# Performance work log

Measured on AMD Instinct MI355X. Metric: run time of the kernel, lower is better.

## Reference

```python
import jax, jax.numpy as jnp
import numpy as np


def _component_indices(d, j):
    # Butterfly component at level j has block size k = d >> j.
    k = d >> j
    half = k // 2
    base = np.arange(d // k) * k                       # block starts
    p = (base[:, None] + np.arange(half)[None, :]).reshape(-1)  # [d//2]
    q = p + half
    return p, q


def butterfly_rotation(thetas, d):
    """Compose m = log2(d) butterfly components: R = B(d,d) @ B(d,d/2) @ ... @ B(d,2).
    thetas: [m, d//2] Givens angles per component (block-major order as in torch)."""
    m = thetas.shape[0]
    R = jnp.eye(d, dtype=thetas.dtype)
    for j in range(m):
        p, q = _component_indices(d, j)
        c = jnp.cos(thetas[j])
        s = jnp.sin(thetas[j])
        C = jnp.eye(d, dtype=thetas.dtype)
        C = C.at[p, p].set(c)
        C = C.at[q, q].set(c)
        C = C.at[p, q].set(-s)
        C = C.at[q, p].set(s)
        R = R @ C
    return R


def setup_inputs() -> dict:
    key = jax.random.key(0)
    ks = jax.random.split(key, 8)
    N, D_IN, D_OUT, R = 16384, 4096, 4096, 1024
    M = 10  # log2(R)
    return {
        "x": jax.random.normal(ks[0], (N, D_IN), dtype=jnp.float32),
        "W": jax.random.normal(ks[1], (D_OUT, D_IN), dtype=jnp.float32) * 0.02,
        "bias": jax.random.normal(ks[2], (D_OUT,), dtype=jnp.float32) * 0.02,
        "U": jax.random.normal(ks[3], (D_OUT, R), dtype=jnp.float32) * 0.02,
        "S": jax.random.uniform(ks[4], (R,), dtype=jnp.float32),
        "V": jax.random.normal(ks[5], (R, D_IN), dtype=jnp.float32) * 0.02,
        "thetas_u": jax.random.normal(ks[6], (M, R // 2), dtype=jnp.float32) * 0.1,
        "thetas_v": jax.random.normal(ks[7], (M, R // 2), dtype=jnp.float32) * 0.1,
    }


def reference(x, W, bias, U, S, V, thetas_u, thetas_v):
    r = S.shape[0]
    R_U = butterfly_rotation(thetas_u, r)  # [r, r]
    R_V = butterfly_rotation(thetas_v, r)  # [r, r]
    # base_layer(x)
    base = x @ W.T + bias                  # [N, out]
    # adapter: x @ V^T @ R_V @ diag(S) @ R_U^T @ U^T
    h = (x @ V.T) @ R_V                    # [N, r]
    h = h * S                              # diag(S)
    delta = (h @ R_U.T) @ U.T              # [N, out]
    return base + delta
```

## Files before the change

### kernel.cpp

```cpp
#include <hip/hip_runtime.h>
#include <cstdint>
#include <cstddef>


typedef __bf16 bf16x8 __attribute__((ext_vector_type(8)));
typedef float floatx4 __attribute__((ext_vector_type(4)));
typedef unsigned short ushortx8 __attribute__((ext_vector_type(8)));

__device__ __forceinline__ unsigned short f2bf(float f) {
    unsigned int u = __builtin_bit_cast(unsigned int, f);
    u += 0x7FFFu + ((u >> 16) & 1u);
    return (unsigned short)(u >> 16);
}

__device__ __forceinline__ void gld_lds16(const void* g, void* l) {
    __builtin_amdgcn_global_load_lds(
        (const __attribute__((address_space(1))) void*)g,
        (__attribute__((address_space(3))) void*)l,
        16, 0, 0);
}

__global__ __launch_bounds__(256) void butterfly_rows_kernel(
    const float* __restrict__ thetas_v, const float* __restrict__ thetas_u,
    const float* __restrict__ S,
    unsigned short* __restrict__ RVsb, unsigned short* __restrict__ RUb)
{
    const int d = 1024;
    __shared__ float w[1024];
    const int b   = blockIdx.x;
    const int mat = b >> 10;
    const int row = b & 1023;
    const float* th = mat ? thetas_u : thetas_v;
    const int t = threadIdx.x;

    for (int i = t; i < d; i += 256) w[i] = (i == row) ? 1.f : 0.f;
    __syncthreads();

    for (int j = 0; j < 10; ++j) {
        const int sh = 9 - j;
        const int halfm1 = (1 << sh) - 1;
        for (int i = t; i < d / 2; i += 256) {
            const int blk = i >> sh;
            const int off = i & halfm1;
            const int p = (blk << (sh + 1)) + off;
            const int q = p + (halfm1 + 1);
            const float theta = th[j * (d / 2) + i];
            float s, c;
            __sincosf(theta, &s, &c);
            const float wp = w[p], wq = w[q];
            w[p] = c * wp + s * wq;
            w[q] = -s * wp + c * wq;
        }
        __syncthreads();
    }

    if (mat == 0) {
        for (int i = t; i < d; i += 256) RVsb[row * d + i] = f2bf(w[i] * S[i]);
    } else {
        for (int i = t; i < d; i += 256) RUb[row * d + i] = f2bf(w[i]);
    }
}

__global__ __launch_bounds__(256) void cvt_f32_bf16_x8(
    const float* __restrict__ src, unsigned short* __restrict__ dst)
{
    const size_t i = ((size_t)blockIdx.x * 256 + threadIdx.x) * 8;
    float4 a = *(const float4*)(src + i);
    float4 b = *(const float4*)(src + i + 4);
    ushortx8 o;
    o[0] = f2bf(a.x); o[1] = f2bf(a.y); o[2] = f2bf(a.z); o[3] = f2bf(a.w);
    o[4] = f2bf(b.x); o[5] = f2bf(b.y); o[6] = f2bf(b.z); o[7] = f2bf(b.w);
    *(ushortx8*)(dst + i) = o;
}

__global__ __launch_bounds__(256) void transpose_to_bf16(
    const float* __restrict__ src, unsigned short* __restrict__ dst,
    int rows, int cols)
{
    __shared__ float tile[32][33];
    const int tx = threadIdx.x & 31, ty = threadIdx.x >> 5;
    const int c0 = blockIdx.x * 32, r0 = blockIdx.y * 32;
    for (int i = 0; i < 32; i += 8)
        tile[ty + i][tx] = src[(size_t)(r0 + ty + i) * cols + c0 + tx];
    __syncthreads();
    for (int i = 0; i < 32; i += 8)
        dst[(size_t)(c0 + ty + i) * rows + r0 + tx] = f2bf(tile[tx][ty + i]);
}

template <int EPI>
__global__ __launch_bounds__(256) void gemm_nt(
    const unsigned short* __restrict__ A,
    const unsigned short* __restrict__ B,
    float* __restrict__ Cf,
    unsigned short* __restrict__ Cb,
    const float* __restrict__ extra,
    int M, int N, int K)
{
    __shared__ __align__(16) unsigned short As[128 * 32];
    __shared__ __align__(16) unsigned short Bs[128 * 32];

    const int tid  = threadIdx.x;
    const int lane = tid & 63;
    const int wave = tid >> 6;
    const int wm = wave >> 1, wn = wave & 1;

    const int m0 = blockIdx.y * 128;
    const int n0 = blockIdx.x * 128;

    const int srow = wave * 32 + (lane >> 2);
    const int scol = (lane & 3) * 8;

    const unsigned short* gA = A + (size_t)(m0 + srow) * K + scol;
    const unsigned short* gB = B + (size_t)(n0 + srow) * K + scol;
    unsigned short* lA = As + wave * 32 * 32;
    unsigned short* lB = Bs + wave * 32 * 32;

    floatx4 acc[4][4];
#pragma unroll
    for (int i = 0; i < 4; ++i)
#pragma unroll
        for (int j = 0; j < 4; ++j) acc[i][j] = (floatx4)0.f;

    const int ar = lane & 15;
    const int ak = (lane >> 4) * 8;

    for (int kk = 0; kk < K; kk += 32) {
        gld_lds16(gA + kk, lA);
        gld_lds16(gA + kk + (size_t)16 * K, lA + 512);
        gld_lds16(gB + kk, lB);
        gld_lds16(gB + kk + (size_t)16 * K, lB + 512);
        __syncthreads();

        bf16x8 af[4], bfr[4];
#pragma unroll
        for (int tm = 0; tm < 4; ++tm)
            af[tm] = __builtin_bit_cast(bf16x8,
                *(const ushortx8*)&As[(wm * 64 + tm * 16 + ar) * 32 + ak]);
#pragma unroll
        for (int tn = 0; tn < 4; ++tn)
            bfr[tn] = __builtin_bit_cast(bf16x8,
                *(const ushortx8*)&Bs[(wn * 64 + tn * 16 + ar) * 32 + ak]);
#pragma unroll
        for (int tm = 0; tm < 4; ++tm)
#pragma unroll
            for (int tn = 0; tn < 4; ++tn)
                acc[tm][tn] = __builtin_amdgcn_mfma_f32_16x16x32_bf16(
                    af[tm], bfr[tn], acc[tm][tn], 0, 0, 0);
        __syncthreads();
    }

#pragma unroll
    for (int tm = 0; tm < 4; ++tm) {
#pragma unroll
        for (int tn = 0; tn < 4; ++tn) {
#pragma unroll
            for (int r = 0; r < 4; ++r) {
                const int row = m0 + wm * 64 + tm * 16 + (lane >> 4) * 4 + r;
                const int col = n0 + wn * 64 + tn * 16 + (lane & 15);
                const float v = acc[tm][tn][r];
                if (EPI == 1) {
                    Cf[(size_t)row * N + col] = v + extra[col];
                } else if (EPI == 2) {
                    Cb[(size_t)row * N + col] = f2bf(v);
                } else {
                    Cb[(size_t)row * N + col] = f2bf(v + extra[(size_t)row * N + col]);
                }
            }
        }
    }
}

template <int EPI>
__global__ __launch_bounds__(512, 2) void gemm256(
    const unsigned short* __restrict__ A,
    const unsigned short* __restrict__ B,
    float* __restrict__ Cf,
    unsigned short* __restrict__ Cb,
    const float* __restrict__ extra,
    int M, int N, int K, int swz_on)
{
    __shared__ __align__(16) unsigned short As[2][256 * 64];
    __shared__ __align__(16) unsigned short Bs[2][256 * 64];

    const int tid  = threadIdx.x;
    const int lane = tid & 63;
    const int wave = tid >> 6;
    const int wm = wave >> 2;
    const int wn = wave & 3;

    int bx = blockIdx.x, by = blockIdx.y;
    if (swz_on) {
        const int gx  = gridDim.x;
        const int nwg = gx * gridDim.y;
        const int f   = by * gx + bx;
        const int g   = (f & 7) * (nwg >> 3) + (f >> 3);
        bx = g % gx;
        by = g / gx;
    }
    const int m0 = by * 256;
    const int n0 = bx * 256;

    const int srow  = tid >> 3;
    const int scolb = (tid & 7) << 4;
    const int scol  = (scolb ^ ((srow & 7) << 4)) >> 1;

    const unsigned short* gA = A + (size_t)(m0 + srow) * K + scol;
    const unsigned short* gB = B + (size_t)(n0 + srow) * K + scol;
    const int ldsoff = wave << 10;
    const size_t rowstep = (size_t)64 * K;

    const int fr   = lane & 15;
    const int fk2  = ((lane >> 4) & 3) << 4;
    const int swz  = (fr & 7) << 4;
    const int ca0  = fk2 ^ swz;
    const int ca1  = (64 + fk2) ^ swz;
    const int arow = (wm * 128 + fr) << 7;
    const int brow = (wn * 64 + fr) << 7;

    floatx4 acc[8][4];
#pragma unroll
    for (int i = 0; i < 8; ++i)
#pragma unroll
        for (int j = 0; j < 4; ++j) acc[i][j] = (floatx4)0.f;

    const int nkt = K >> 6;

    {
        char* la = (char*)&As[0][0] + ldsoff;
        char* lb = (char*)&Bs[0][0] + ldsoff;
#pragma unroll
        for (int j = 0; j < 4; ++j) gld_lds16(gA + j * rowstep, la + j * 8192);
#pragma unroll
        for (int j = 0; j < 4; ++j) gld_lds16(gB + j * rowstep, lb + j * 8192);
    }

    for (int t = 0; t < nkt; ++t) {
        if (t + 1 < nkt) {
            const unsigned short* a = gA + (size_t)(t + 1) * 64;
            const unsigned short* b = gB + (size_t)(t + 1) * 64;
            char* la = (char*)&As[(t + 1) & 1][0] + ldsoff;
            char* lb = (char*)&Bs[(t + 1) & 1][0] + ldsoff;
#pragma unroll
            for (int j = 0; j < 4; ++j) gld_lds16(a + j * rowstep, la + j * 8192);
#pragma unroll
            for (int j = 0; j < 4; ++j) gld_lds16(b + j * rowstep, lb + j * 8192);
            __builtin_amdgcn_sched_barrier(0);
            asm volatile("s_waitcnt vmcnt(8)" ::: "memory");
        } else {
            asm volatile("s_waitcnt vmcnt(0)" ::: "memory");
        }
        __builtin_amdgcn_s_barrier();
        __builtin_amdgcn_sched_barrier(0);

        const char* ab = (const char*)&As[t & 1][0];
        const char* bb = (const char*)&Bs[t & 1][0];

        bf16x8 af[4][2], b0[2][2], b1[2][2];

#pragma unroll
        for (int mf = 0; mf < 4; ++mf) {
            af[mf][0] = __builtin_bit_cast(bf16x8, *(const ushortx8*)(ab + arow + (mf << 11) + ca0));
            af[mf][1] = __builtin_bit_cast(bf16x8, *(const ushortx8*)(ab + arow + (mf << 11) + ca1));
        }
#pragma unroll
        for (int nf = 0; nf < 2; ++nf) {
            b0[nf][0] = __builtin_bit_cast(bf16x8, *(const ushortx8*)(bb + brow + (nf << 11) + ca0));
            b0[nf][1] = __builtin_bit_cast(bf16x8, *(const ushortx8*)(bb + brow + (nf << 11) + ca1));
        }
        __builtin_amdgcn_s_setprio(1);
#pragma unroll
        for (int mf = 0; mf < 4; ++mf)
#pragma unroll
            for (int nf = 0; nf < 2; ++nf) {
                acc[mf][nf] = __builtin_amdgcn_mfma_f32_16x16x32_bf16(af[mf][0], b0[nf][0], acc[mf][nf], 0, 0, 0);
                acc[mf][nf] = __builtin_amdgcn_mfma_f32_16x16x32_bf16(af[mf][1], b0[nf][1], acc[mf][nf], 0, 0, 0);
            }
        __builtin_amdgcn_s_setprio(0);

#pragma unroll
        for (int nf = 0; nf < 2; ++nf) {
            b1[nf][0] = __builtin_bit_cast(bf16x8, *(const ushortx8*)(bb + brow + 4096 + (nf << 11) + ca0));
            b1[nf][1] = __builtin_bit_cast(bf16x8, *(const ushortx8*)(bb + brow + 4096 + (nf << 11) + ca1));
        }
        __builtin_amdgcn_s_setprio(1);
#pragma unroll
        for (int mf = 0; mf < 4; ++mf)
#pragma unroll
            for (int nf = 0; nf < 2; ++nf) {
                acc[mf][2 + nf] = __builtin_amdgcn_mfma_f32_16x16x32_bf16(af[mf][0], b1[nf][0], acc[mf][2 + nf], 0, 0, 0);
                acc[mf][2 + nf] = __builtin_amdgcn_mfma_f32_16x16x32_bf16(af[mf][1], b1[nf][1], acc[mf][2 + nf], 0, 0, 0);
            }
        __builtin_amdgcn_s_setprio(0);

#pragma unroll
        for (int mf = 0; mf < 4; ++mf) {
            af[mf][0] = __builtin_bit_cast(bf16x8, *(const ushortx8*)(ab + arow + 8192 + (mf << 11) + ca0));
            af[mf][1] = __builtin_bit_cast(bf16x8, *(const ushortx8*)(ab + arow + 8192 + (mf << 11) + ca1));
        }
        __builtin_amdgcn_s_setprio(1);
#pragma unroll
        for (int mf = 0; mf < 4; ++mf)
#pragma unroll
            for (int nf = 0; nf < 2; ++nf) {
                acc[4 + mf][2 + nf] = __builtin_amdgcn_mfma_f32_16x16x32_bf16(af[mf][0], b1[nf][0], acc[4 + mf][2 + nf], 0, 0, 0);
                acc[4 + mf][2 + nf] = __builtin_amdgcn_mfma_f32_16x16x32_bf16(af[mf][1], b1[nf][1], acc[4 + mf][2 + nf], 0, 0, 0);
            }
        __builtin_amdgcn_s_setprio(0);

#pragma unroll
        for (int nf = 0; nf < 2; ++nf) {
            b0[nf][0] = __builtin_bit_cast(bf16x8, *(const ushortx8*)(bb + brow + (nf << 11) + ca0));
            b0[nf][1] = __builtin_bit_cast(bf16x8, *(const ushortx8*)(bb + brow + (nf << 11) + ca1));
        }
        __builtin_amdgcn_s_setprio(1);
#pragma unroll
        for (int mf = 0; mf < 4; ++mf)
#pragma unroll
            for (int nf = 0; nf < 2; ++nf) {
                acc[4 + mf][nf] = __builtin_amdgcn_mfma_f32_16x16x32_bf16(af[mf][0], b0[nf][0], acc[4 + mf][nf], 0, 0, 0);
                acc[4 + mf][nf] = __builtin_amdgcn_mfma_f32_16x16x32_bf16(af[mf][1], b0[nf][1], acc[4 + mf][nf], 0, 0, 0);
            }
        __builtin_amdgcn_s_setprio(0);

        __builtin_amdgcn_sched_barrier(0);
        asm volatile("" ::: "memory");
        __builtin_amdgcn_s_barrier();
    }

    const int er = wm * 128 + ((lane >> 4) << 2);
    const int ec = wn * 64 + (lane & 15);
#pragma unroll
    for (int mfg = 0; mfg < 8; ++mfg) {
#pragma unroll
        for (int nfg = 0; nfg < 4; ++nfg) {
#pragma unroll
            for (int r = 0; r < 4; ++r) {
                const int row = m0 + er + mfg * 16 + r;
                const int col = n0 + ec + nfg * 16;
                const float v = acc[mfg][nfg][r];
                if (EPI == 1) {
                    Cf[(size_t)row * N + col] = v + extra[col];
                } else {
                    Cb[(size_t)row * N + col] = f2bf(v + extra[(size_t)row * N + col]);
                }
            }
        }
    }
    (void)M;
}

extern "C" void kernel_launch(void* const* d_in, const int* in_sizes, int n_in,
                              void* d_out, int out_size, void* d_ws, size_t ws_size,
                              hipStream_t stream)
{
    const int NB = 16384, DIN = 4096, DOUT = 4096, R = 1024;

    const float* x    = (const float*)d_in[0];
    const float* W    = (const float*)d_in[1];
    const float* bias = (const float*)d_in[2];
    const float* U    = (const float*)d_in[3];
    const float* S    = (const float*)d_in[4];
    const float* V    = (const float*)d_in[5];
    const float* th_u = (const float*)d_in[6];
    const float* th_v = (const float*)d_in[7];
    float* out = (float*)d_out;

    char* ws = (char*)d_ws;
    size_t off = 0;
    auto alloc = [&](size_t bytes) {
        char* p = ws + off;
        off += (bytes + 255) & ~(size_t)255;
        return p;
    };
    unsigned short* Xb   = (unsigned short*)alloc((size_t)NB * DIN * 2);
    unsigned short* Wctb = (unsigned short*)alloc((size_t)DOUT * DIN * 2);
    unsigned short* RVsb = (unsigned short*)alloc((size_t)R * R * 2);
    unsigned short* RUb  = (unsigned short*)alloc((size_t)R * R * 2);
    unsigned short* Tb   = (unsigned short*)alloc((size_t)R * R * 2);
    unsigned short* Ub   = (unsigned short*)alloc((size_t)DOUT * R * 2);
    unsigned short* Gb   = (unsigned short*)alloc((size_t)DOUT * R * 2);
    unsigned short* Vtb  = (unsigned short*)alloc((size_t)DIN * R * 2);
    if (off > ws_size) return;

    butterfly_rows_kernel<<<2048, 256, 0, stream>>>(th_v, th_u, S, RVsb, RUb);

    cvt_f32_bf16_x8<<<(NB * (size_t)DIN) / 2048, 256, 0, stream>>>(x, Xb);
    cvt_f32_bf16_x8<<<((size_t)DOUT * R) / 2048, 256, 0, stream>>>(U, Ub);
    transpose_to_bf16<<<dim3(DIN / 32, R / 32), 256, 0, stream>>>(V, Vtb, R, DIN);

    gemm_nt<2><<<dim3(R / 128, R / 128), 256, 0, stream>>>(
        RVsb, RUb, nullptr, Tb, nullptr, R, R, R);

    gemm_nt<2><<<dim3(R / 128, DOUT / 128), 256, 0, stream>>>(
        Ub, Tb, nullptr, Gb, nullptr, DOUT, R, R);

    gemm256<3><<<dim3(DIN / 256, DOUT / 256), 512, 0, stream>>>(
        Gb, Vtb, nullptr, Wctb, W, DOUT, DIN, R, 0);

    gemm256<1><<<dim3(DOUT / 256, NB / 256), 512, 0, stream>>>(
        Xb, Wctb, out, nullptr, bias, NB, DOUT, DIN, 1);
}
```

Baseline: 1.202 ms.

## Split 256x256 GEMM tile into quadrant halves with staggered per-half prefetch

The 256x256 bf16 GEMM kernel now keeps A and B in LDS as two 128-row halves per buffer. Each wave's fragments are remapped to interleaved 64x32 sub-tiles inside each half. Loads for the next k-tile are issued one half at a time between the four MFMA phases, with partial vmcnt waits and barriers, so global-to-LDS traffic overlaps compute more finely and each phase only waits for the half it needs. This adds several extra workgroup barriers per k-iteration and more complex wait-count bookkeeping, which could cause stalls or ordering hazards.

Measured after the change: 1.142 ms. 5.0% less time.

```diff
diff --git a/kernel.cpp b/kernel.cpp
--- a/kernel.cpp
+++ b/kernel.cpp
@@ -19,6 +19,12 @@
         (__attribute__((address_space(3))) void*)l,
         16, 0, 0);
 }
+
+__device__ __forceinline__ bf16x8 ldsv(const char* p) {
+    return __builtin_bit_cast(bf16x8, *(const ushortx8*)p);
+}
+
+#define MFMA_BF16(a, b, c) __builtin_amdgcn_mfma_f32_16x16x32_bf16((a), (b), (c), 0, 0, 0)
 
 __global__ __launch_bounds__(256) void butterfly_rows_kernel(
     const float* __restrict__ thetas_v, const float* __restrict__ thetas_u,
@@ -144,8 +150,7 @@
         for (int tm = 0; tm < 4; ++tm)
 #pragma unroll
             for (int tn = 0; tn < 4; ++tn)
-                acc[tm][tn] = __builtin_amdgcn_mfma_f32_16x16x32_bf16(
-                    af[tm], bfr[tn], acc[tm][tn], 0, 0, 0);
+                acc[tm][tn] = MFMA_BF16(af[tm], bfr[tn], acc[tm][tn]);
         __syncthreads();
     }
 
@@ -179,8 +184,8 @@
     const float* __restrict__ extra,
     int M, int N, int K, int swz_on)
 {
-    __shared__ __align__(16) unsigned short As[2][256 * 64];
-    __shared__ __align__(16) unsigned short Bs[2][256 * 64];
+    __shared__ __align__(16) unsigned short As[2][2][128][64];
+    __shared__ __align__(16) unsigned short Bs[2][2][128][64];
 
     const int tid  = threadIdx.x;
     const int lane = tid & 63;
@@ -203,19 +208,32 @@
     const int srow  = tid >> 3;
     const int scolb = (tid & 7) << 4;
     const int scol  = (scolb ^ ((srow & 7) << 4)) >> 1;
-
     const unsigned short* gA = A + (size_t)(m0 + srow) * K + scol;
     const unsigned short* gB = B + (size_t)(n0 + srow) * K + scol;
-    const int ldsoff = wave << 10;
-    const size_t rowstep = (size_t)64 * K;
-
-    const int fr   = lane & 15;
-    const int fk2  = ((lane >> 4) & 3) << 4;
-    const int swz  = (fr & 7) << 4;
-    const int ca0  = fk2 ^ swz;
-    const int ca1  = (64 + fk2) ^ swz;
-    const int arow = (wm * 128 + fr) << 7;
-    const int brow = (wn * 64 + fr) << 7;
+    char* lA = (char*)As + (wave << 10);
+    char* lB = (char*)Bs + (wave << 10);
+    const size_t rs64 = (size_t)64 * K;
+
+    auto stA = [&](int t1, int h) {
+        const unsigned short* s = gA + (size_t)h * 2 * rs64 + (size_t)t1 * 64;
+        char* l = lA + (t1 & 1) * 32768 + h * 16384;
+        gld_lds16(s, l);
+        gld_lds16(s + rs64, l + 8192);
+    };
+    auto stB = [&](int t1, int h) {
+        const unsigned short* s = gB + (size_t)h * 2 * rs64 + (size_t)t1 * 64;
+        char* l = lB + (t1 & 1) * 32768 + h * 16384;
+        gld_lds16(s, l);
+        gld_lds16(s + rs64, l + 8192);
+    };
+
+    const int fr  = lane & 15;
+    const int kg  = lane >> 4;
+    const int swz = (fr & 7) << 4;
+    const int ca0 = (kg << 4) ^ swz;
+    const int ca1 = (64 + (kg << 4)) ^ swz;
+    const int arb = (wm * 64 + fr) * 128;
+    const int brb = (wn * 32 + fr) * 128;
 
     floatx4 acc[8][4];
 #pragma unroll
@@ -225,127 +243,127 @@
 
     const int nkt = K >> 6;
 
-    {
-        char* la = (char*)&As[0][0] + ldsoff;
-        char* lb = (char*)&Bs[0][0] + ldsoff;
-#pragma unroll
-        for (int j = 0; j < 4; ++j) gld_lds16(gA + j * rowstep, la + j * 8192);
-#pragma unroll
-        for (int j = 0; j < 4; ++j) gld_lds16(gB + j * rowstep, lb + j * 8192);
-    }
+    stA(0, 0); stB(0, 0); stB(0, 1); stA(0, 1);
+    asm volatile("s_waitcnt vmcnt(4)" ::: "memory");
+    __builtin_amdgcn_s_barrier();
+    __builtin_amdgcn_sched_barrier(0);
 
     for (int t = 0; t < nkt; ++t) {
-        if (t + 1 < nkt) {
-            const unsigned short* a = gA + (size_t)(t + 1) * 64;
-            const unsigned short* b = gB + (size_t)(t + 1) * 64;
-            char* la = (char*)&As[(t + 1) & 1][0] + ldsoff;
-            char* lb = (char*)&Bs[(t + 1) & 1][0] + ldsoff;
-#pragma unroll
-            for (int j = 0; j < 4; ++j) gld_lds16(a + j * rowstep, la + j * 8192);
-#pragma unroll
-            for (int j = 0; j < 4; ++j) gld_lds16(b + j * rowstep, lb + j * 8192);
-            __builtin_amdgcn_sched_barrier(0);
-            asm volatile("s_waitcnt vmcnt(8)" ::: "memory");
-        } else {
-            asm volatile("s_waitcnt vmcnt(0)" ::: "memory");
-        }
-        __builtin_amdgcn_s_barrier();
-        __builtin_amdgcn_sched_barrier(0);
-
-        const char* ab = (const char*)&As[t & 1][0];
-        const char* bb = (const char*)&Bs[t & 1][0];
+        const bool stg = (t + 1 < nkt);
+        const char* Ad = (const char*)As + (t & 1) * 32768;
+        const char* Bd = (const char*)Bs + (t & 1) * 32768;
 
         bf16x8 af[4][2], b0[2][2], b1[2][2];
 
 #pragma unroll
         for (int mf = 0; mf < 4; ++mf) {
-            af[mf][0] = __builtin_bit_cast(bf16x8, *(const ushortx8*)(ab + arow + (mf << 11) + ca0));
-            af[mf][1] = __builtin_bit_cast(bf16x8, *(const ushortx8*)(ab + arow + (mf << 11) + ca1));
+            af[mf][0] = ldsv(Ad + arb + mf * 2048 + ca0);
+            af[mf][1] = ldsv(Ad + arb + mf * 2048 + ca1);
         }
 #pragma unroll
         for (int nf = 0; nf < 2; ++nf) {
-            b0[nf][0] = __builtin_bit_cast(bf16x8, *(const ushortx8*)(bb + brow + (nf << 11) + ca0));
-            b0[nf][1] = __builtin_bit_cast(bf16x8, *(const ushortx8*)(bb + brow + (nf << 11) + ca1));
-        }
+            b0[nf][0] = ldsv(Bd + brb + nf * 2048 + ca0);
+            b0[nf][1] = ldsv(Bd + brb + nf * 2048 + ca1);
+        }
+        if (stg) { stA(t + 1, 0); asm volatile("s_waitcnt vmcnt(4)" ::: "memory"); }
+        else     {                asm volatile("s_waitcnt vmcnt(2)" ::: "memory"); }
+        __builtin_amdgcn_s_barrier();
+        asm volatile("s_waitcnt lgkmcnt(0)" ::: "memory");
+        __builtin_amdgcn_sched_barrier(0);
         __builtin_amdgcn_s_setprio(1);
 #pragma unroll
         for (int mf = 0; mf < 4; ++mf)
 #pragma unroll
             for (int nf = 0; nf < 2; ++nf) {
-                acc[mf][nf] = __builtin_amdgcn_mfma_f32_16x16x32_bf16(af[mf][0], b0[nf][0], acc[mf][nf], 0, 0, 0);
-                acc[mf][nf] = __builtin_amdgcn_mfma_f32_16x16x32_bf16(af[mf][1], b0[nf][1], acc[mf][nf], 0, 0, 0);
+                acc[mf][nf] = MFMA_BF16(af[mf][0], b0[nf][0], acc[mf][nf]);
+                acc[mf][nf] = MFMA_BF16(af[mf][1], b0[nf][1], acc[mf][nf]);
             }
         __builtin_amdgcn_s_setprio(0);
+        __builtin_amdgcn_s_barrier();
+        __builtin_amdgcn_sched_barrier(0);
 
 #pragma unroll
         for (int nf = 0; nf < 2; ++nf) {
-            b1[nf][0] = __builtin_bit_cast(bf16x8, *(const ushortx8*)(bb + brow + 4096 + (nf << 11) + ca0));
-            b1[nf][1] = __builtin_bit_cast(bf16x8, *(const ushortx8*)(bb + brow + 4096 + (nf << 11) + ca1));
-        }
+            b1[nf][0] = ldsv(Bd + 16384 + brb + nf * 2048 + ca0);
+            b1[nf][1] = ldsv(Bd + 16384 + brb + nf * 2048 + ca1);
+        }
+        if (stg) { stB(t + 1, 0); asm volatile("s_waitcnt vmcnt(4)" ::: "memory"); }
+        else     {                asm volatile("s_waitcnt vmcnt(0)" ::: "memory"); }
+        __builtin_amdgcn_s_barrier();
+        asm volatile("s_waitcnt lgkmcnt(0)" ::: "memory");
+        __builtin_amdgcn_sched_barrier(0);
         __builtin_amdgcn_s_setprio(1);
 #pragma unroll
         for (int mf = 0; mf < 4; ++mf)
 #pragma unroll
             for (int nf = 0; nf < 2; ++nf) {
-                acc[mf][2 + nf] = __builtin_amdgcn_mfma_f32_16x16x32_bf16(af[mf][0], b1[nf][0], acc[mf][2 + nf], 0, 0, 0);
-                acc[mf][2 + nf] = __builtin_amdgcn_mfma_f32_16x16x32_bf16(af[mf][1], b1[nf][1], acc[mf][2 + nf], 0, 0, 0);
+                acc[mf][2 + nf] = MFMA_BF16(af[mf][0], b1[nf][0], acc[mf][2 + nf]);
+                acc[mf][2 + nf] = MFMA_BF16(af[mf][1], b1[nf][1], acc[mf][2 + nf]);
             }
         __builtin_amdgcn_s_setprio(0);
+        __builtin_amdgcn_s_barrier();
+        __builtin_amdgcn_sched_barrier(0);
 
 #pragma unroll
         for (int mf = 0; mf < 4; ++mf) {
-            af[mf][0] = __builtin_bit_cast(bf16x8, *(const ushortx8*)(ab + arow + 8192 + (mf << 11) + ca0));
-            af[mf][1] = __builtin_bit_cast(bf16x8, *(const ushortx8*)(ab + arow + 8192 + (mf << 11) + ca1));
-        }
+            af[mf][0] = ldsv(Ad + 16384 + arb + mf * 2048 + ca0);
+            af[mf][1] = ldsv(Ad + 16384 + arb + mf * 2048 + ca1);
+        }
+        if (stg) stB(t + 1, 1);
+        asm volatile("" ::: "memory");
+        __builtin_amdgcn_s_barrier();
+        asm volatile("s_waitcnt lgkmcnt(0)" ::: "memory");
+        __builtin_amdgcn_sched_barrier(0);
         __builtin_amdgcn_s_setprio(1);
 #pragma unroll
         for (int mf = 0; mf < 4; ++mf)
 #pragma unroll
             for (int nf = 0; nf < 2; ++nf) {
-                acc[4 + mf][2 + nf] = __builtin_amdgcn_mfma_f32_16x16x32_bf16(af[mf][0], b1[nf][0], acc[4 + mf][2 + nf], 0, 0, 0);
-                acc[4 + mf][2 + nf] = __builtin_amdgcn_mfma_f32_16x16x32_bf16(af[mf][1], b1[nf][1], acc[4 + mf][2 + nf], 0, 0, 0);
+                acc[4 + mf][2 + nf] = MFMA_BF16(af[mf][0], b1[nf][0], acc[4 + mf][2 + nf]);
+                acc[4 + mf][2 + nf] = MFMA_BF16(af[mf][1], b1[nf][1], acc[4 + mf][2 + nf]);
             }
         __builtin_amdgcn_s_setprio(0);
-
-#pragma unroll
-        for (int nf = 0; nf < 2; ++nf) {
-            b0[nf][0] = __builtin_bit_cast(bf16x8, *(const ushortx8*)(bb + brow + (nf << 11) + ca0));
-            b0[nf][1] = __builtin_bit_cast(bf16x8, *(const ushortx8*)(bb + brow + (nf << 11) + ca1));
-        }
+        __builtin_amdgcn_s_barrier();
+        __builtin_amdgcn_sched_barrier(0);
+
+        if (stg) { stA(t + 1, 1); asm volatile("s_waitcnt vmcnt(4)" ::: "memory"); }
+        else     {                asm volatile("" ::: "memory"); }
+        __builtin_amdgcn_s_barrier();
+        __builtin_amdgcn_sched_barrier(0);
         __builtin_amdgcn_s_setprio(1);
 #pragma unroll
         for (int mf = 0; mf < 4; ++mf)
 #pragma unroll
             for (int nf = 0; nf < 2; ++nf) {
-                acc[4 + mf][nf] = __builtin_amdgcn_mfma_f32_16x16x32_bf16(af[mf][0], b0[nf][0], acc[4 + mf][nf], 0, 0, 0);
-                acc[4 + mf][nf] = __builtin_amdgcn_mfma_f32_16x16x32_bf16(af[mf][1], b0[nf][1], acc[4 + mf][nf], 0, 0, 0);
+                acc[4 + mf][nf] = MFMA_BF16(af[mf][0], b0[nf][0], acc[4 + mf][nf]);
+                acc[4 + mf][nf] = MFMA_BF16(af[mf][1], b0[nf][1], acc[4 + mf][nf]);
             }
         __builtin_amdgcn_s_setprio(0);
-
-        __builtin_amdgcn_sched_barrier(0);
-        asm volatile("" ::: "memory");
-        __builtin_amdgcn_s_barrier();
-    }
-
-    const int er = wm * 128 + ((lane >> 4) << 2);
-    const int ec = wn * 64 + (lane & 15);
-#pragma unroll
-    for (int mfg = 0; mfg < 8; ++mfg) {
-#pragma unroll
-        for (int nfg = 0; nfg < 4; ++nfg) {
-#pragma unroll
-            for (int r = 0; r < 4; ++r) {
-                const int row = m0 + er + mfg * 16 + r;
-                const int col = n0 + ec + nfg * 16;
-                const float v = acc[mfg][nfg][r];
-                if (EPI == 1) {
-                    Cf[(size_t)row * N + col] = v + extra[col];
-                } else {
-                    Cb[(size_t)row * N + col] = f2bf(v + extra[(size_t)row * N + col]);
-                }
-            }
-        }
-    }
+        __builtin_amdgcn_s_barrier();
+        __builtin_amdgcn_sched_barrier(0);
+    }
+
+    const int er4 = (lane >> 4) << 2;
+    const int ec  = lane & 15;
+#pragma unroll
+    for (int Mq = 0; Mq < 2; ++Mq)
+#pragma unroll
+        for (int mf = 0; mf < 4; ++mf)
+#pragma unroll
+            for (int Nq = 0; Nq < 2; ++Nq)
+#pragma unroll
+                for (int nf = 0; nf < 2; ++nf)
+#pragma unroll
+                    for (int r = 0; r < 4; ++r) {
+                        const int row = m0 + Mq * 128 + wm * 64 + mf * 16 + er4 + r;
+                        const int col = n0 + Nq * 128 + wn * 32 + nf * 16 + ec;
+                        const float v = acc[Mq * 4 + mf][Nq * 2 + nf][r];
+                        if (EPI == 1) {
+                            Cf[(size_t)row * N + col] = v + extra[col];
+                        } else {
+                            Cb[(size_t)row * N + col] = f2bf(v + extra[(size_t)row * N + col]);
+                        }
+                    }
     (void)M;
 }
 
```
